# Optimization experiments

Hardware: AMD Instinct MI355X
Metric: run time of the kernel (lower is better)

The kernel has to match this reference:

```python
import jax, jax.numpy as jnp
import numpy as np

D = 128          # lattice edge (Z = Y = X = 128)
S = 8            # state_size
H = 16           # hidden_size
IN = 7 * S       # own state + 6 neighbor states = 56


def setup_inputs() -> dict:
    key = jax.random.key(0)
    k0, k1, k2 = jax.random.split(key, 3)
    N = D * D * D
    states = jax.random.normal(k0, (N, S), dtype=jnp.float32)
    W1 = jax.random.normal(k1, (IN, H), dtype=jnp.float32) * (1.0 / np.sqrt(IN))
    b1 = jnp.zeros((H,), dtype=jnp.float32)
    W2 = jax.random.normal(k2, (H, S), dtype=jnp.float32) * (1.0 / np.sqrt(H))
    b2 = jnp.zeros((S,), dtype=jnp.float32)
    return {"states": states, "W1": W1, "b1": b1, "W2": W2, "b2": b2}


def reference(states, W1, b1, W2, b2):
    # linear index = z*(X*Y) + y*X + x  ->  grid layout (Z, Y, X, S)
    g = states.reshape(D, D, D, S)
    # 6-neighbor gather with periodic boundary (NEIGHBOR_DIRECTIONS order:
    # (-1,0,0),(1,0,0),(0,-1,0),(0,1,0),(0,0,-1),(0,0,1)); x->axis2, y->axis1, z->axis0.
    # roll(+1) along an axis fetches the neighbor in the -1 direction.
    nbrs = [
        jnp.roll(g,  1, axis=2),  # x-1
        jnp.roll(g, -1, axis=2),  # x+1
        jnp.roll(g,  1, axis=1),  # y-1
        jnp.roll(g, -1, axis=1),  # y+1
        jnp.roll(g,  1, axis=0),  # z-1
        jnp.roll(g, -1, axis=0),  # z+1
    ]
    inp = jnp.concatenate([g] + nbrs, axis=-1)          # (Z, Y, X, 56)
    h = jnp.tanh(jnp.einsum('zyxi,ih->zyxh', inp, W1) + b1)
    out = jnp.einsum('zyxh,hs->zyxs', h, W2) + b2        # (Z, Y, X, 8)
    return out.reshape(-1, S)
```

## Files before the change

### kernel.cpp

```cpp
#include <hip/hip_runtime.h>

#define DIM 128
#define SLOT_STRIDE 2096
#define PLANE_STRIDE (6 * SLOT_STRIDE)

typedef __attribute__((ext_vector_type(8))) short bf16x8;
typedef __attribute__((ext_vector_type(4))) float f32x4;
typedef __attribute__((ext_vector_type(4))) unsigned int u32x4;

static __device__ __forceinline__ unsigned short f2bf_rne(float f) {
    union { float f; unsigned int i; } c; c.f = f;
    unsigned int u = c.i;
    return (unsigned short)((u + 0x7fffu + ((u >> 16) & 1u)) >> 16);
}
static __device__ __forceinline__ unsigned int fbits(float f) {
    union { float f; unsigned int i; } c; c.f = f; return c.i;
}
static __device__ __forceinline__ unsigned int pack_bf16_rne(float lo, float hi) {
    unsigned int ul = fbits(lo), uh = fbits(hi);
    unsigned int tl = ul + 0x7fffu + ((ul >> 16) & 1u);
    unsigned int th = uh + 0x7fffu + ((uh >> 16) & 1u);
    return __builtin_amdgcn_perm(th, tl, 0x07060302u);
}

struct Frags {
    bf16x8 w1h0, w1h1, w2h;
    f32x4 b1v, b2v;
};

static __device__ __forceinline__ void build_frags(
    const float* W1, const float* b1, const float* W2, const float* b2,
    int col, int quad, Frags& F)
{
#pragma unroll
    for (int j = 0; j < 8; ++j) {
        int k0 = quad * 8 + j;
        F.w1h0[j] = (short)f2bf_rne(W1[k0 * 16 + col]);
        int k1 = 32 + quad * 8 + j;
        F.w1h1[j] = (short)f2bf_rne((k1 < 56) ? W1[k1 * 16 + col] : 0.0f);
        float w2 = (j < 4 && col < 8) ? W2[(quad * 4 + j) * 8 + col] : 0.0f;
        F.w2h[j] = (short)f2bf_rne(w2);
    }
#pragma unroll
    for (int r = 0; r < 4; ++r) {
        F.b1v[r] = b1[quad * 4 + r];
        F.b2v[r] = (quad < 2) ? b2[quad * 4 + r] : 0.0f;
    }
}

__global__ __launch_bounds__(64) void setup_kernel(
    const float* __restrict__ W1, const float* __restrict__ b1,
    const float* __restrict__ W2, const float* __restrict__ b2,
    u32x4* __restrict__ ws)
{
    const int lane = threadIdx.x;
    Frags F;
    build_frags(W1, b1, W2, b2, lane & 15, lane >> 4, F);
    union { bf16x8 v; u32x4 u; } c;
    c.v = F.w1h0; ws[0 * 64 + lane] = c.u;
    c.v = F.w1h1; ws[1 * 64 + lane] = c.u;
    c.v = F.w2h;  ws[2 * 64 + lane] = c.u;
    union { f32x4 v; u32x4 u; } b;
    b.v = F.b1v; ws[3 * 64 + lane] = b.u;
    b.v = F.b2v; ws[4 * 64 + lane] = b.u;
}

template<bool USE_WS>
__global__ __launch_bounds__(256, 4) void lattice_kernel(
    const float* __restrict__ states,
    const float* __restrict__ W1, const float* __restrict__ b1,
    const float* __restrict__ W2, const float* __restrict__ b2,
    float* __restrict__ out, const u32x4* __restrict__ ws)
{
    __shared__ __align__(16) unsigned char lds[3 * PLANE_STRIDE];

    const int tid  = threadIdx.x;
    const int lane = tid & 63;
    const int w    = __builtin_amdgcn_readfirstlane(tid >> 6);
    const int col  = lane & 15;
    const int quad = lane >> 4;

    Frags F;
    if (USE_WS) {
        union { u32x4 u; bf16x8 v; } c;
        c.u = ws[0 * 64 + lane]; F.w1h0 = c.v;
        c.u = ws[1 * 64 + lane]; F.w1h1 = c.v;
        c.u = ws[2 * 64 + lane]; F.w2h  = c.v;
        union { u32x4 u; f32x4 v; } b;
        b.u = ws[3 * 64 + lane]; F.b1v = b.v;
        b.u = ws[4 * 64 + lane]; F.b2v = b.v;
    } else {
        build_frags(W1, b1, W2, b2, col, quad, F);
    }

    const int bI   = blockIdx.x;
    const int slab = bI & 7;
    const int inr  = bI >> 3;
    const int z0   = ((slab << 2) + (inr >> 5)) << 2;
    const int y0   = (inr & 31) << 2;

    auto issue_plane = [&](int zp, f32x4* a, f32x4* b) {
#pragma unroll
        for (int i = 0; i < 3; ++i) {
            const int tk   = w * 3 + i;
            const int r    = tk >> 1;
            const int half = tk & 1;
            const int yr   = (y0 - 1 + r) & 127;
            const float* g = states +
                ((size_t)((((unsigned)(zp & 127)) << 14) + (yr << 7) + (half << 6)) << 3);
            a[i] = *(const f32x4*)(g + (lane << 3));
            b[i] = *(const f32x4*)(g + (lane << 3) + 4);
        }
    };
    auto write_plane = [&](int buf, const f32x4* a, const f32x4* b) {
#pragma unroll
        for (int i = 0; i < 3; ++i) {
            const int tk   = w * 3 + i;
            const int r    = tk >> 1;
            const int half = tk & 1;
            u32x4 p;
            p[0] = __builtin_amdgcn_perm(fbits(a[i][1]), fbits(a[i][0]), 0x07060302u);
            p[1] = __builtin_amdgcn_perm(fbits(a[i][3]), fbits(a[i][2]), 0x07060302u);
            p[2] = __builtin_amdgcn_perm(fbits(b[i][1]), fbits(b[i][0]), 0x07060302u);
            p[3] = __builtin_amdgcn_perm(fbits(b[i][3]), fbits(b[i][2]), 0x07060302u);
            unsigned char* base = lds + buf * PLANE_STRIDE + r * SLOT_STRIDE;
            *(u32x4*)(base + ((half * 64 + lane + 1) << 4)) = p;
            if (half == 0 && lane == 0)  *(u32x4*)(base + 2064) = p;
            if (half == 1 && lane == 63) *(u32x4*)(base) = p;
        }
    };

    f32x4 gA[3], gB[3], hA[3], hB[3];
    issue_plane(z0 - 1, gA, gB);
    issue_plane(z0,     hA, hB);
    write_plane(0, gA, gB);
    issue_plane(z0 + 1, gA, gB);
    write_plane(1, hA, hB);
    write_plane(2, gA, gB);
    __syncthreads();

    const int dxA  = (quad == 1) ? -1 : (quad == 2) ? 1 : 0;
    const int rA   = (quad == 3) ? w : w + 1;
    const int rB   = (quad == 0) ? w + 2 : w + 1;
    const int offA = rA * SLOT_STRIDE + ((col + dxA + 1) << 4);
    const int offB = rB * SLOT_STRIDE + ((col + 1) << 4);

#pragma unroll
    for (int s = 0; s < 4; ++s) {
        const int zc = z0 + s;
        if (s < 3) issue_plane(zc + 2, gA, gB);

        const int bufZm = s % 3, bufZ = (s + 1) % 3, bufZp = (s + 2) % 3;
        const unsigned char* pA = lds + bufZ * PLANE_STRIDE + offA;
        const int bB = (quad == 1) ? bufZm : (quad == 2) ? bufZp : bufZ;
        const unsigned char* pB = lds + bB * PLANE_STRIDE + offB;

        float* pO = out + (size_t)(((zc << 14) + ((y0 + w) << 7) + col) * 8 + quad * 4);

#pragma unroll
        for (int i = 0; i < 8; ++i) {
            bf16x8 s0f = *(const bf16x8*)(pA + (i << 8));
            bf16x8 s1f = *(const bf16x8*)(pB + (i << 8));

            f32x4 acc = F.b1v;
            acc = __builtin_amdgcn_mfma_f32_16x16x32_bf16(F.w1h0, s0f, acc, 0, 0, 0);
            acc = __builtin_amdgcn_mfma_f32_16x16x32_bf16(F.w1h1, s1f, acc, 0, 0, 0);

            float h0t, h1t, h2t, h3t;
            {
                float e;
                e = __expf(2.0f * acc[0]); h0t = 1.0f - 2.0f * __builtin_amdgcn_rcpf(e + 1.0f);
                e = __expf(2.0f * acc[1]); h1t = 1.0f - 2.0f * __builtin_amdgcn_rcpf(e + 1.0f);
                e = __expf(2.0f * acc[2]); h2t = 1.0f - 2.0f * __builtin_amdgcn_rcpf(e + 1.0f);
                e = __expf(2.0f * acc[3]); h3t = 1.0f - 2.0f * __builtin_amdgcn_rcpf(e + 1.0f);
            }
            union { bf16x8 v; unsigned int u[4]; } hf;
            hf.u[0] = pack_bf16_rne(h0t, h1t);
            hf.u[1] = pack_bf16_rne(h2t, h3t);
            hf.u[2] = 0u;
            hf.u[3] = 0u;

            f32x4 acc2 = F.b2v;
            acc2 = __builtin_amdgcn_mfma_f32_16x16x32_bf16(F.w2h, hf.v, acc2, 0, 0, 0);

            if (quad < 2) {
                __builtin_nontemporal_store(acc2, (f32x4*)(pO + (i << 7)));
            }
        }

        __syncthreads();
        if (s < 3) {
            write_plane(bufZm, gA, gB);
            __syncthreads();
        }
    }
}

extern "C" void kernel_launch(void* const* d_in, const int* in_sizes, int n_in,
                              void* d_out, int out_size, void* d_ws, size_t ws_size,
                              hipStream_t stream) {
    const float* states = (const float*)d_in[0];
    const float* W1     = (const float*)d_in[1];
    const float* b1     = (const float*)d_in[2];
    const float* W2     = (const float*)d_in[3];
    const float* b2     = (const float*)d_in[4];
    float* out          = (float*)d_out;

    const bool use_ws = ws_size >= (size_t)(5 * 64 * 16);
    if (use_ws) {
        hipLaunchKernelGGL(setup_kernel, dim3(1), dim3(64), 0, stream,
                           W1, b1, W2, b2, (u32x4*)d_ws);
        hipLaunchKernelGGL((lattice_kernel<true>), dim3(1024), dim3(256), 0, stream,
                           states, W1, b1, W2, b2, out, (const u32x4*)d_ws);
    } else {
        hipLaunchKernelGGL((lattice_kernel<false>), dim3(1024), dim3(256), 0, stream,
                           states, W1, b1, W2, b2, out, (const u32x4*)d_ws);
    }
}
```

Before: 122.5 us.

## Use four-plane LDS ring to overlap plane writes with compute and halve barriers

```diff
diff --git a/kernel.cpp b/kernel.cpp
--- a/kernel.cpp
+++ b/kernel.cpp
@@ -66,13 +66,13 @@
 }
 
 template<bool USE_WS>
-__global__ __launch_bounds__(256, 4) void lattice_kernel(
+__global__ __launch_bounds__(256, 3) void lattice_kernel(
     const float* __restrict__ states,
     const float* __restrict__ W1, const float* __restrict__ b1,
     const float* __restrict__ W2, const float* __restrict__ b2,
     float* __restrict__ out, const u32x4* __restrict__ ws)
 {
-    __shared__ __align__(16) unsigned char lds[3 * PLANE_STRIDE];
+    __shared__ __align__(16) unsigned char lds[4 * PLANE_STRIDE];
 
     const int tid  = threadIdx.x;
     const int lane = tid & 63;
@@ -130,31 +130,16 @@
         }
     };
 
-    f32x4 gA[3], gB[3], hA[3], hB[3];
-    issue_plane(z0 - 1, gA, gB);
-    issue_plane(z0,     hA, hB);
-    write_plane(0, gA, gB);
-    issue_plane(z0 + 1, gA, gB);
-    write_plane(1, hA, hB);
-    write_plane(2, gA, gB);
-    __syncthreads();
-
     const int dxA  = (quad == 1) ? -1 : (quad == 2) ? 1 : 0;
     const int rA   = (quad == 3) ? w : w + 1;
     const int rB   = (quad == 0) ? w + 2 : w + 1;
     const int offA = rA * SLOT_STRIDE + ((col + dxA + 1) << 4);
     const int offB = rB * SLOT_STRIDE + ((col + 1) << 4);
 
-#pragma unroll
-    for (int s = 0; s < 4; ++s) {
-        const int zc = z0 + s;
-        if (s < 3) issue_plane(zc + 2, gA, gB);
-
-        const int bufZm = s % 3, bufZ = (s + 1) % 3, bufZp = (s + 2) % 3;
+    auto compute_step = [&](int zc, int bufZm, int bufZ, int bufZp) {
         const unsigned char* pA = lds + bufZ * PLANE_STRIDE + offA;
         const int bB = (quad == 1) ? bufZm : (quad == 2) ? bufZp : bufZ;
         const unsigned char* pB = lds + bB * PLANE_STRIDE + offB;
-
         float* pO = out + (size_t)(((zc << 14) + ((y0 + w) << 7) + col) * 8 + quad * 4);
 
 #pragma unroll
@@ -187,13 +172,30 @@
                 __builtin_nontemporal_store(acc2, (f32x4*)(pO + (i << 7)));
             }
         }
-
-        __syncthreads();
-        if (s < 3) {
-            write_plane(bufZm, gA, gB);
-            __syncthreads();
-        }
-    }
+    };
+
+    f32x4 Aa[3], Ab[3], Ba[3], Bb[3];
+    issue_plane(z0 - 1, Aa, Ab);
+    issue_plane(z0,     Ba, Bb);
+    write_plane(0, Aa, Ab);
+    issue_plane(z0 + 1, Aa, Ab);
+    write_plane(1, Ba, Bb);
+    issue_plane(z0 + 2, Ba, Bb);
+    write_plane(2, Aa, Ab);
+    __syncthreads();
+
+    issue_plane(z0 + 3, Aa, Ab);
+    write_plane(3, Ba, Bb);
+    compute_step(z0 + 0, 0, 1, 2);
+    __syncthreads();
+    issue_plane(z0 + 4, Ba, Bb);
+    write_plane(0, Aa, Ab);
+    compute_step(z0 + 1, 1, 2, 3);
+    __syncthreads();
+    write_plane(1, Ba, Bb);
+    compute_step(z0 + 2, 2, 3, 0);
+    __syncthreads();
+    compute_step(z0 + 3, 3, 0, 1);
 }
 
 extern "C" void kernel_launch(void* const* d_in, const int* in_sizes, int n_in,
```

New measurement: 122.0 us. No clear change (-0.4%).
